# Kernel optimization log

Hardware: AMD Instinct MI355X
Metric: run time of the kernel (lower is better)

The kernel has to match this reference:

```python
import jax, jax.numpy as jnp
import numpy as np

N = 50000      # nodes
E = 800000     # edges (before self-loops)
IN = 128       # in_channels
HID = 32       # hidden_channels
H = 4          # heads (hidden layers)
H_LAST = 6     # heads of final conv (concat=False -> mean)
OUT = 2        # out_channels
NEG = 0.2      # LeakyReLU slope in GATConv


def setup_inputs() -> dict:
    key = jax.random.key(0)
    ks = jax.random.split(key, 24)
    r = lambda k, s, sc=0.1: (jax.random.normal(k, s, jnp.float32) * sc)
    inp = {
        "x": jax.random.normal(ks[0], (N, IN), jnp.float32),
        "edge_index": jax.random.randint(ks[1], (2, E), 0, N, dtype=jnp.int32),
        "edge_attr": jax.random.normal(ks[2], (E, 1), jnp.float32),  # ignored by GATConv (edge_dim=None)
        # layer 0: GATConv(IN -> HID, heads=H, concat) + Linear(IN -> HID*H)
        "c0_W": r(ks[3], (IN, H * HID)), "c0_as": r(ks[4], (H, HID)), "c0_ad": r(ks[5], (H, HID)), "c0_b": jnp.zeros((H * HID,), jnp.float32),
        "l0_W": r(ks[6], (IN, H * HID)), "l0_b": jnp.zeros((H * HID,), jnp.float32),
        # layer 1 (middle): GATConv(HID*H -> HID, heads=H) + Linear(HID*H -> HID*H)
        "c1_W": r(ks[7], (H * HID, H * HID)), "c1_as": r(ks[8], (H, HID)), "c1_ad": r(ks[9], (H, HID)), "c1_b": jnp.zeros((H * HID,), jnp.float32),
        "l1_W": r(ks[10], (H * HID, H * HID)), "l1_b": jnp.zeros((H * HID,), jnp.float32),
        # layer 2 (last): GATConv(HID*H -> OUT, heads=H_LAST, concat=False) + Linear(HID*H -> OUT)
        "c2_W": r(ks[11], (H * HID, H_LAST * OUT)), "c2_as": r(ks[12], (H_LAST, OUT)), "c2_ad": r(ks[13], (H_LAST, OUT)), "c2_b": jnp.zeros((OUT,), jnp.float32),
        "l2_W": r(ks[14], (H * HID, OUT)), "l2_b": jnp.zeros((OUT,), jnp.float32),
    }
    return inp


def gat_conv(x, src, dst, W, a_src, a_dst, b, heads, ch, concat):
    n = x.shape[0]
    xw = (x @ W).reshape(n, heads, ch)                      # [N,H,C]
    al_s = jnp.einsum('nhc,hc->nh', xw, a_src)              # [N,H]
    al_d = jnp.einsum('nhc,hc->nh', xw, a_dst)
    alpha = jax.nn.leaky_relu(al_s[src] + al_d[dst], NEG)   # [E,H]
    # segment softmax over edges sharing the same destination node
    m = jax.ops.segment_max(alpha, dst, num_segments=n)
    e = jnp.exp(alpha - m[dst])
    s = jax.ops.segment_sum(e, dst, num_segments=n)
    coef = e / s[dst]                                       # [E,H]
    out = jax.ops.segment_sum(xw[src] * coef[:, :, None], dst, num_segments=n)  # [N,H,C]
    out = out.reshape(n, heads * ch) if concat else out.mean(axis=1)
    return out + b


def reference(x, edge_index, edge_attr,
              c0_W, c0_as, c0_ad, c0_b, l0_W, l0_b,
              c1_W, c1_as, c1_ad, c1_b, l1_W, l1_b,
              c2_W, c2_as, c2_ad, c2_b, l2_W, l2_b):
    n = x.shape[0]
    loops = jnp.arange(n, dtype=edge_index.dtype)  # GATConv add_self_loops=True
    src = jnp.concatenate([edge_index[0], loops])
    dst = jnp.concatenate([edge_index[1], loops])
    # edge_attr is ignored: GATConv built without edge_dim has lin_edge=None
    h = jax.nn.relu(gat_conv(x, src, dst, c0_W, c0_as, c0_ad, c0_b, H, HID, True) + x @ l0_W + l0_b)
    h = jax.nn.relu(gat_conv(h, src, dst, c1_W, c1_as, c1_ad, c1_b, H, HID, True) + h @ l1_W + l1_b)
    out = gat_conv(h, src, dst, c2_W, c2_as, c2_ad, c2_b, H_LAST, OUT, False) + h @ l2_W + l2_b
    return out
```

## Files before the change

kernel.cpp:

```cpp
#include <hip/hip_runtime.h>
#include <hip/hip_bf16.h>


#define NEG_SLOPE 0.2f
#define SC_CHUNK 4096
#define CAP 64

typedef __attribute__((ext_vector_type(8))) short short8;
typedef __attribute__((ext_vector_type(4))) float floatx4;

static __device__ __forceinline__ float leaky(float x) {
    return x > 0.f ? x : NEG_SLOPE * x;
}

static __device__ __forceinline__ unsigned short f2bf(float f) {
    unsigned int u = __float_as_uint(f);
    u = (u + 0x7fffu + ((u >> 16) & 1u)) >> 16;
    return (unsigned short)u;
}

static __device__ __forceinline__ unsigned int pack_bf2(float lo, float hi) {
    return (unsigned int)f2bf(lo) | ((unsigned int)f2bf(hi) << 16);
}

static __device__ __forceinline__ float bflo(unsigned int u) {
    return __uint_as_float(u << 16);
}
static __device__ __forceinline__ float bfhi(unsigned int u) {
    return __uint_as_float(u & 0xffff0000u);
}

__global__ __launch_bounds__(256) void k_bucket(
    const int* __restrict__ ei, int E, int N, int rs,
    int* __restrict__ cnt, int* __restrict__ col) {
    int lo = blockIdx.x * rs, hi = lo + rs;
    int base = blockIdx.y * SC_CHUNK;
    int ET = E + N;
#pragma unroll 4
    for (int o = threadIdx.x; o < SC_CHUNK; o += 256) {
        int e = base + o;
        if (e >= ET) break;
        int d = (e < E) ? ei[E + e] : (e - E);
        if (d < lo || d >= hi) continue;
        int s = (e < E) ? ei[e] : d;
        int pos = atomicAdd(&cnt[d], 1);
        if (pos < CAP) col[(d << 6) + pos] = s;
    }
}


__global__ void k_conv_x(const float* __restrict__ x, unsigned short* __restrict__ Ab,
                         int N, int Mpad) {
    int t = blockIdx.x * 256 + threadIdx.x;
    if (t >= Mpad * 32) return;
    int r = t >> 5;
    float4 v = make_float4(0.f, 0.f, 0.f, 0.f);
    if (r < N) v = ((const float4*)x)[t];
    ushort4 o;
    o.x = f2bf(v.x); o.y = f2bf(v.y); o.z = f2bf(v.z); o.w = f2bf(v.w);
    ((ushort4*)Ab)[t] = o;
}

__global__ void k_conv_w(const float* W0, unsigned short* T0,
                         const float* W1, unsigned short* T1,
                         const float* W2, unsigned short* T2,
                         const float* W3, unsigned short* T3,
                         const float* c2W, const float* l2W, unsigned short* WT5) {
    int t = blockIdx.x * 256 + threadIdx.x;
    if (blockIdx.y == 4) {
        if (t >= 2048) return;
        int n = t >> 7, k = t & 127;
        float v = 0.f;
        if (n < 12) v = c2W[k * 12 + n];
        else if (n < 14) v = l2W[k * 2 + (n - 12)];
        WT5[n * 128 + k] = f2bf(v);
        return;
    }
    const float* W; unsigned short* T;
    switch (blockIdx.y) {
        case 0: W = W0; T = T0; break;
        case 1: W = W1; T = T1; break;
        case 2: W = W2; T = T2; break;
        default: W = W3; T = T3; break;
    }
    int n = t >> 7, k = t & 127;
    T[n * 128 + k] = f2bf(W[k * 128 + n]);
}

__global__ __launch_bounds__(256) void k_gemm_mfma(
    const unsigned short* __restrict__ Ab,
    const unsigned short* __restrict__ W1T,
    unsigned int* __restrict__ XWb,
    const float* __restrict__ a_s, const float* __restrict__ a_d,
    float4* __restrict__ ALS4, float4* __restrict__ ALD4,
    const unsigned short* __restrict__ W2T,
    const float* __restrict__ b2,
    unsigned short* __restrict__ Hsb,
    int M) {
    int which = blockIdx.y;
    const unsigned short* WT = which ? W2T : W1T;
    int row0 = blockIdx.x * 64;
    int w = threadIdx.x >> 6, lane = threadIdx.x & 63;
    int m = lane & 15, q = lane >> 4;

    const short8* A8 = (const short8*)Ab;
    const short8* W8 = (const short8*)WT;

    floatx4 acc[8];
#pragma unroll
    for (int ct = 0; ct < 8; ct++) acc[ct] = (floatx4){0.f, 0.f, 0.f, 0.f};

    int arow = row0 + w * 16 + m;
#pragma unroll
    for (int ks = 0; ks < 4; ks++) {
        short8 afrag = A8[arow * 16 + ks * 4 + q];
#pragma unroll
        for (int ct = 0; ct < 8; ct++) {
            short8 bfrag = W8[(ct * 16 + m) * 16 + ks * 4 + q];
            acc[ct] = __builtin_amdgcn_mfma_f32_16x16x32_bf16(afrag, bfrag, acc[ct], 0, 0, 0);
        }
    }

    int crow0 = row0 + w * 16 + q * 4;
    if (which) {
#pragma unroll
        for (int ct = 0; ct < 8; ct++) {
            int gc = ct * 16 + m;
            float bias = b2[gc];
#pragma unroll
            for (int r = 0; r < 4; r++) {
                int gr = crow0 + r;
                if (gr < M) Hsb[gr * 128 + gc] = f2bf(acc[ct][r] + bias);
            }
        }
    } else {
#pragma unroll
        for (int ct = 0; ct < 4; ct++) {
#pragma unroll
            for (int r = 0; r < 4; r++) {
                int gr = crow0 + r;
                if (gr < M)
                    XWb[gr * 64 + ct * 16 + m] = pack_bf2(acc[ct][r], acc[ct + 4][r]);
            }
        }
        float sv[4][4], dv[4][4];
#pragma unroll
        for (int h = 0; h < 4; h++) {
            float as0 = a_s[h * 32 + m], as1 = a_s[h * 32 + 16 + m];
            float ad0 = a_d[h * 32 + m], ad1 = a_d[h * 32 + 16 + m];
#pragma unroll
            for (int r = 0; r < 4; r++) {
                sv[h][r] = acc[2 * h][r] * as0 + acc[2 * h + 1][r] * as1;
                dv[h][r] = acc[2 * h][r] * ad0 + acc[2 * h + 1][r] * ad1;
            }
        }
#pragma unroll
        for (int off = 8; off >= 1; off >>= 1) {
#pragma unroll
            for (int h = 0; h < 4; h++)
#pragma unroll
                for (int r = 0; r < 4; r++) {
                    sv[h][r] += __shfl_xor(sv[h][r], off);
                    dv[h][r] += __shfl_xor(dv[h][r], off);
                }
        }
        if (m == 0) {
#pragma unroll
            for (int r = 0; r < 4; r++) {
                int gr = crow0 + r;
                if (gr < M) {
                    ALS4[gr] = make_float4(sv[0][r], sv[1][r], sv[2][r], sv[3][r]);
                    ALD4[gr] = make_float4(dv[0][r], dv[1][r], dv[2][r], dv[3][r]);
                }
            }
        }
    }
}

__global__ __launch_bounds__(256) void k_gemm_small(
    const unsigned short* __restrict__ Ab,
    const unsigned short* __restrict__ WT5,
    const float* __restrict__ c2as, const float* __restrict__ c2ad,
    const float* __restrict__ l2b,
    float* __restrict__ L2D, float* __restrict__ ALD2,
    float* __restrict__ out, int M) {
    int w = threadIdx.x >> 6, lane = threadIdx.x & 63;
    int m = lane & 15, q = lane >> 4;
    const short8* A8 = (const short8*)Ab;
    const short8* W8 = (const short8*)WT5;
    floatx4 acc = (floatx4){0.f, 0.f, 0.f, 0.f};
    int arow = blockIdx.x * 64 + w * 16 + m;
#pragma unroll
    for (int ks = 0; ks < 4; ks++) {
        short8 afrag = A8[arow * 16 + ks * 4 + q];
        short8 bfrag = W8[m * 16 + ks * 4 + q];
        acc = __builtin_amdgcn_mfma_f32_16x16x32_bf16(afrag, bfrag, acc, 0, 0, 0);
    }
    float asm_ = (m < 12) ? c2as[m] : 0.f;
    float adm  = (m < 12) ? c2ad[m] : 0.f;
    int crow0 = blockIdx.x * 64 + w * 16 + q * 4;
    float sc[4], dc[4];
#pragma unroll
    for (int r = 0; r < 4; r++) {
        sc[r] = acc[r] * asm_;
        dc[r] = acc[r] * adm;
    }
#pragma unroll
    for (int r = 0; r < 4; r++) {
        sc[r] += __shfl_xor(sc[r], 1);
        dc[r] += __shfl_xor(dc[r], 1);
    }
#pragma unroll
    for (int r = 0; r < 4; r++) {
        int gr = crow0 + r;
        if (gr >= M) continue;
        if (m < 12) {
            L2D[gr * 20 + m] = acc[r];
            if ((m & 1) == 0) {
                int h = m >> 1;
                L2D[gr * 20 + 12 + h] = sc[r];
                ALD2[gr * 8 + h] = dc[r];
            }
        } else if (m == 12) {
            out[gr * 2 + 0] = acc[r] + l2b[0];
        } else if (m == 13) {
            out[gr * 2 + 1] = acc[r] + l2b[1];
        }
    }
}

__global__ __launch_bounds__(256) void k_agg4(
    const int* __restrict__ cntv, const int* __restrict__ col,
    const uint4* __restrict__ XWb4,
    const float4* __restrict__ ALS4, const float4* __restrict__ ALD4,
    const float* __restrict__ cb,
    const unsigned short* __restrict__ Hsb, unsigned short* __restrict__ Hb, int N) {
    int wid = threadIdx.x >> 6, lane = threadIdx.x & 63;
    int node = blockIdx.x * 4 + wid;
    if (node >= N) return;
    int deg = cntv[node];
    if (deg > CAP) deg = CAP;
    int start = node << 6;
    int gq = lane >> 4, g = lane & 15;
    int hA = g >> 3;
    int cval = col[start + lane];
    float4 ad = ALD4[node];
    float adA = hA ? ad.y : ad.x;
    float adB = hA ? ad.w : ad.z;

    float a0 = 0.f, a1 = 0.f, a2 = 0.f, a3 = 0.f;
    float b0 = 0.f, b1 = 0.f, b2 = 0.f, b3 = 0.f;
    float sA = 0.f, sB = 0.f;

#define EDGE(sv)                                                       \
    {                                                                  \
        float4 as = ALS4[sv];                                          \
        uint4 u = XWb4[(size_t)(sv) * 16 + g];                         \
        float eA = __expf(leaky((hA ? as.y : as.x) + adA));            \
        float eB = __expf(leaky((hA ? as.w : as.z) + adB));            \
        sA += eA; sB += eB;                                            \
        a0 += eA * bflo(u.x); b0 += eB * bfhi(u.x);                    \
        a1 += eA * bflo(u.y); b1 += eB * bfhi(u.y);                    \
        a2 += eA * bflo(u.z); b2 += eB * bfhi(u.z);                    \
        a3 += eA * bflo(u.w); b3 += eB * bfhi(u.w);                    \
    }

    int i = 0;
    for (; i + 16 <= deg; i += 16) {
        int s0 = __shfl(cval, i + gq);
        int s1 = __shfl(cval, i + 4 + gq);
        int s2 = __shfl(cval, i + 8 + gq);
        int s3 = __shfl(cval, i + 12 + gq);
        EDGE(s0) EDGE(s1) EDGE(s2) EDGE(s3)
    }
    for (; i + 4 <= deg; i += 4) {
        int s0 = __shfl(cval, i + gq);
        EDGE(s0)
    }
    int rem = deg - i;
    if (rem > 0) {
        int s0 = __shfl(cval, i + (gq < rem ? gq : 0));
        if (gq < rem) EDGE(s0)
    }
#undef EDGE

#define RED2(v) { v += __shfl_xor(v, 16); v += __shfl_xor(v, 32); }
    RED2(sA) RED2(sB)
    RED2(a0) RED2(a1) RED2(a2) RED2(a3)
    RED2(b0) RED2(b1) RED2(b2) RED2(b3)
#undef RED2

    if (gq == 0) {
        float invA = 1.f / sA, invB = 1.f / sB;
        float4 cl = ((const float4*)cb)[g];
        float4 ch = ((const float4*)cb)[g + 16];
        uint2 skl = ((const uint2*)(Hsb + node * 128))[g];
        uint2 skh = ((const uint2*)(Hsb + node * 128 + 64))[g];
        float v0 = a0 * invA + cl.x + bflo(skl.x);
        float v1 = a1 * invA + cl.y + bfhi(skl.x);
        float v2 = a2 * invA + cl.z + bflo(skl.y);
        float v3 = a3 * invA + cl.w + bfhi(skl.y);
        float w0 = b0 * invB + ch.x + bflo(skh.x);
        float w1 = b1 * invB + ch.y + bfhi(skh.x);
        float w2 = b2 * invB + ch.z + bflo(skh.y);
        float w3 = b3 * invB + ch.w + bfhi(skh.y);
        v0 = v0 > 0.f ? v0 : 0.f;  v1 = v1 > 0.f ? v1 : 0.f;
        v2 = v2 > 0.f ? v2 : 0.f;  v3 = v3 > 0.f ? v3 : 0.f;
        w0 = w0 > 0.f ? w0 : 0.f;  w1 = w1 > 0.f ? w1 : 0.f;
        w2 = w2 > 0.f ? w2 : 0.f;  w3 = w3 > 0.f ? w3 : 0.f;
        uint2 ol, oh;
        ol.x = pack_bf2(v0, v1); ol.y = pack_bf2(v2, v3);
        oh.x = pack_bf2(w0, w1); oh.y = pack_bf2(w2, w3);
        ((uint2*)(Hb + node * 128))[g] = ol;
        ((uint2*)(Hb + node * 128 + 64))[g] = oh;
    }
}

__global__ __launch_bounds__(256) void k_agg2(
    const int* __restrict__ cntv, const int* __restrict__ col,
    const float4* __restrict__ L2D4,
    const float* __restrict__ ALD2,
    const float* __restrict__ c2b,
    float* __restrict__ out, int N) {
    int g = threadIdx.x >> 4, l = threadIdx.x & 15;
    int node = blockIdx.x * 16 + g;
    if (node >= N) return;
    int deg = cntv[node];
    if (deg > CAP) deg = CAP;
    int start = node << 6;

    int c0 = (l      < deg) ? col[start + l]      : -1;
    int c1 = (l + 16 < deg) ? col[start + l + 16] : -1;
    int c2 = (l + 32 < deg) ? col[start + l + 32] : -1;
    int c3 = (l + 48 < deg) ? col[start + l + 48] : -1;

    float ald[6];
    {
        float4 d03 = *(const float4*)(ALD2 + node * 8);
        float2 d45 = *(const float2*)(ALD2 + node * 8 + 4);
        ald[0] = d03.x; ald[1] = d03.y; ald[2] = d03.z; ald[3] = d03.w;
        ald[4] = d45.x; ald[5] = d45.y;
    }

    float se[6], a0[6], a1[6];
#pragma unroll
    for (int h = 0; h < 6; h++) { se[h] = 0.f; a0[h] = 0.f; a1[h] = 0.f; }

#define EDGE2(sv)                                                          \
    if ((sv) >= 0) {                                                       \
        float4 x03 = L2D4[(sv) * 5 + 0];                                   \
        float4 x47 = L2D4[(sv) * 5 + 1];                                   \
        float4 x8b = L2D4[(sv) * 5 + 2];                                   \
        float4 as03 = L2D4[(sv) * 5 + 3];                                  \
        float4 as45 = L2D4[(sv) * 5 + 4];                                  \
        float als[6] = {as03.x, as03.y, as03.z, as03.w, as45.x, as45.y};   \
        float xw[12] = {x03.x, x03.y, x03.z, x03.w, x47.x, x47.y, x47.z,   \
                        x47.w, x8b.x, x8b.y, x8b.z, x8b.w};                \
        _Pragma("unroll")                                                  \
        for (int h = 0; h < 6; h++) {                                      \
            float e = __expf(leaky(als[h] + ald[h]));                      \
            se[h] += e;                                                    \
            a0[h] += e * xw[2 * h];                                        \
            a1[h] += e * xw[2 * h + 1];                                    \
        }                                                                  \
    }

    EDGE2(c0) EDGE2(c1) EDGE2(c2) EDGE2(c3)
#undef EDGE2

#pragma unroll
    for (int m = 8; m >= 1; m >>= 1) {
#pragma unroll
        for (int h = 0; h < 6; h++) {
            se[h] += __shfl_xor(se[h], m);
            a0[h] += __shfl_xor(a0[h], m);
            a1[h] += __shfl_xor(a1[h], m);
        }
    }
    if (l == 0) {
        float o0 = 0.f, o1 = 0.f;
#pragma unroll
        for (int h = 0; h < 6; h++) {
            float inv = 1.f / se[h];
            o0 += a0[h] * inv;
            o1 += a1[h] * inv;
        }
        out[node * 2 + 0] += o0 * (1.f / 6.f) + c2b[0];
        out[node * 2 + 1] += o1 * (1.f / 6.f) + c2b[1];
    }
}


extern "C" void kernel_launch(void* const* d_in, const int* in_sizes, int n_in,
                              void* d_out, int out_size, void* d_ws, size_t ws_size,
                              hipStream_t stream) {
    const float* x   = (const float*)d_in[0];
    const int* ei    = (const int*)d_in[1];
    const float* c0W = (const float*)d_in[3];
    const float* c0as = (const float*)d_in[4];
    const float* c0ad = (const float*)d_in[5];
    const float* c0b = (const float*)d_in[6];
    const float* l0W = (const float*)d_in[7];
    const float* l0b = (const float*)d_in[8];
    const float* c1W = (const float*)d_in[9];
    const float* c1as = (const float*)d_in[10];
    const float* c1ad = (const float*)d_in[11];
    const float* c1b = (const float*)d_in[12];
    const float* l1W = (const float*)d_in[13];
    const float* l1b = (const float*)d_in[14];
    const float* c2W = (const float*)d_in[15];
    const float* c2as = (const float*)d_in[16];
    const float* c2ad = (const float*)d_in[17];
    const float* c2b = (const float*)d_in[18];
    const float* l2W = (const float*)d_in[19];
    const float* l2b = (const float*)d_in[20];
    float* out = (float*)d_out;

    const int N = in_sizes[0] / 128;
    const int E = in_sizes[1] / 2;
    const int ET = E + N;
    const int Mpad = (N + 63) & ~63;

    char* p = (char*)d_ws;
    auto alloc = [&](size_t bytes) -> void* {
        void* r = (void*)p;
        p += (bytes + 255) & ~(size_t)255;
        return r;
    };
    unsigned short* Hsb = (unsigned short*)alloc((size_t)N * 128 * 2);
    unsigned int* XWb = (unsigned int*)alloc((size_t)N * 64 * 4);
    unsigned short* Ab = (unsigned short*)alloc((size_t)Mpad * 128 * 2);
    unsigned short* W1T = (unsigned short*)alloc(128 * 128 * 2);
    unsigned short* W2T = (unsigned short*)alloc(128 * 128 * 2);
    unsigned short* W3T = (unsigned short*)alloc(128 * 128 * 2);
    unsigned short* W4T = (unsigned short*)alloc(128 * 128 * 2);
    unsigned short* WT5 = (unsigned short*)alloc(16 * 128 * 2);
    float* ALS = (float*)alloc((size_t)N * 4 * 4);
    float* ALD = (float*)alloc((size_t)N * 8 * 4);
    float* L2D = (float*)alloc((size_t)N * 20 * 4);
    int* cnt    = (int*)alloc((size_t)N * 4);
    int* col    = (int*)alloc((size_t)N * CAP * 4);

    hipMemsetAsync(cnt, 0, (size_t)N * 4, stream);
    int rs = (N + 7) / 8;
    dim3 bgrid(8, (ET + SC_CHUNK - 1) / SC_CHUNK);
    k_bucket<<<bgrid, 256, 0, stream>>>(ei, E, N, rs, cnt, col);

    k_conv_x<<<(Mpad * 32 + 255) / 256, 256, 0, stream>>>(x, Ab, N, Mpad);
    dim3 wgrid(64, 5);
    k_conv_w<<<wgrid, 256, 0, stream>>>(c0W, W1T, l0W, W2T, c1W, W3T, l1W, W4T,
                                        c2W, l2W, WT5);

    dim3 ggrid(Mpad / 64, 2);
    int nwb = (N + 3) / 4;

    k_gemm_mfma<<<ggrid, 256, 0, stream>>>(Ab, W1T, XWb, c0as, c0ad,
                                           (float4*)ALS, (float4*)ALD,
                                           W2T, l0b, Hsb, N);
    k_agg4<<<nwb, 256, 0, stream>>>(cnt, col, (const uint4*)XWb,
                                    (const float4*)ALS, (const float4*)ALD,
                                    c0b, Hsb, Ab, N);

    k_gemm_mfma<<<ggrid, 256, 0, stream>>>(Ab, W3T, XWb, c1as, c1ad,
                                           (float4*)ALS, (float4*)ALD,
                                           W4T, l1b, Hsb, N);
    k_agg4<<<nwb, 256, 0, stream>>>(cnt, col, (const uint4*)XWb,
                                    (const float4*)ALS, (const float4*)ALD,
                                    c1b, Hsb, Ab, N);

    k_gemm_small<<<Mpad / 64, 256, 0, stream>>>(Ab, WT5, c2as, c2ad, l2b,
                                                L2D, ALD, out, N);
    k_agg2<<<(N + 15) / 16, 256, 0, stream>>>(cnt, col, (const float4*)L2D,
                                              ALD, c2b, out, N);
}
```

Measured before the change: 332.1 us.

## Fuse weight conversion into bucketing and x conversion into first GEMM

Weight transposition and bf16 conversion now run in an extra row of blocks of the edge-bucketing kernel, and the standalone x-to-bf16 kernel is removed. The first GEMM instead reads fp32 x directly and converts the A fragments in registers. This drops two kernel launches and one full write and read of the converted x. The aggregation kernel also issues its bias and skip-connection loads before the edge loop so their latency overlaps the gather. The cost is that the first GEMM reads twice as many input bytes, and x is read once per column block.

```diff
diff --git a/kernel.cpp b/kernel.cpp
--- a/kernel.cpp
+++ b/kernel.cpp
@@ -30,9 +30,44 @@
     return __uint_as_float(u & 0xffff0000u);
 }
 
+static __device__ __forceinline__ short8 frag_from_f32(const float* p) {
+    float4 f0 = ((const float4*)p)[0];
+    float4 f1 = ((const float4*)p)[1];
+    short8 r;
+    r[0] = (short)f2bf(f0.x); r[1] = (short)f2bf(f0.y);
+    r[2] = (short)f2bf(f0.z); r[3] = (short)f2bf(f0.w);
+    r[4] = (short)f2bf(f1.x); r[5] = (short)f2bf(f1.y);
+    r[6] = (short)f2bf(f1.z); r[7] = (short)f2bf(f1.w);
+    return r;
+}
+
 __global__ __launch_bounds__(256) void k_bucket(
     const int* __restrict__ ei, int E, int N, int rs,
-    int* __restrict__ cnt, int* __restrict__ col) {
+    int* __restrict__ cnt, int* __restrict__ col,
+    const float* __restrict__ W0, unsigned short* __restrict__ T0,
+    const float* __restrict__ W1, unsigned short* __restrict__ T1,
+    const float* __restrict__ W2, unsigned short* __restrict__ T2,
+    const float* __restrict__ W3, unsigned short* __restrict__ T3,
+    const float* __restrict__ c2W, const float* __restrict__ l2W,
+    unsigned short* __restrict__ WT5) {
+    if (blockIdx.y == gridDim.y - 1) {
+        int tid = blockIdx.x * 256 + threadIdx.x;
+        for (int j = tid; j < 65536; j += 2048) {
+            int wsel = j >> 14, t = j & 16383;
+            int n = t >> 7, k = t & 127;
+            const float* W = (wsel == 0) ? W0 : (wsel == 1) ? W1 : (wsel == 2) ? W2 : W3;
+            unsigned short* T = (wsel == 0) ? T0 : (wsel == 1) ? T1 : (wsel == 2) ? T2 : T3;
+            T[n * 128 + k] = f2bf(W[k * 128 + n]);
+        }
+        {
+            int n = tid >> 7, k = tid & 127;
+            float v = 0.f;
+            if (n < 12) v = c2W[k * 12 + n];
+            else if (n < 14) v = l2W[k * 2 + (n - 12)];
+            WT5[n * 128 + k] = f2bf(v);
+        }
+        return;
+    }
     int lo = blockIdx.x * rs, hi = lo + rs;
     int base = blockIdx.y * SC_CHUNK;
     int ET = E + N;
@@ -48,46 +83,8 @@
     }
 }
 
-
-__global__ void k_conv_x(const float* __restrict__ x, unsigned short* __restrict__ Ab,
-                         int N, int Mpad) {
-    int t = blockIdx.x * 256 + threadIdx.x;
-    if (t >= Mpad * 32) return;
-    int r = t >> 5;
-    float4 v = make_float4(0.f, 0.f, 0.f, 0.f);
-    if (r < N) v = ((const float4*)x)[t];
-    ushort4 o;
-    o.x = f2bf(v.x); o.y = f2bf(v.y); o.z = f2bf(v.z); o.w = f2bf(v.w);
-    ((ushort4*)Ab)[t] = o;
-}
-
-__global__ void k_conv_w(const float* W0, unsigned short* T0,
-                         const float* W1, unsigned short* T1,
-                         const float* W2, unsigned short* T2,
-                         const float* W3, unsigned short* T3,
-                         const float* c2W, const float* l2W, unsigned short* WT5) {
-    int t = blockIdx.x * 256 + threadIdx.x;
-    if (blockIdx.y == 4) {
-        if (t >= 2048) return;
-        int n = t >> 7, k = t & 127;
-        float v = 0.f;
-        if (n < 12) v = c2W[k * 12 + n];
-        else if (n < 14) v = l2W[k * 2 + (n - 12)];
-        WT5[n * 128 + k] = f2bf(v);
-        return;
-    }
-    const float* W; unsigned short* T;
-    switch (blockIdx.y) {
-        case 0: W = W0; T = T0; break;
-        case 1: W = W1; T = T1; break;
-        case 2: W = W2; T = T2; break;
-        default: W = W3; T = T3; break;
-    }
-    int n = t >> 7, k = t & 127;
-    T[n * 128 + k] = f2bf(W[k * 128 + n]);
-}
-
 __global__ __launch_bounds__(256) void k_gemm_mfma(
+    const float* __restrict__ x0,
     const unsigned short* __restrict__ Ab,
     const unsigned short* __restrict__ W1T,
     unsigned int* __restrict__ XWb,
@@ -111,9 +108,11 @@
     for (int ct = 0; ct < 8; ct++) acc[ct] = (floatx4){0.f, 0.f, 0.f, 0.f};
 
     int arow = row0 + w * 16 + m;
+    int lrow = (arow < M) ? arow : (M - 1);
 #pragma unroll
     for (int ks = 0; ks < 4; ks++) {
-        short8 afrag = A8[arow * 16 + ks * 4 + q];
+        short8 afrag = x0 ? frag_from_f32(x0 + (size_t)lrow * 128 + (ks * 4 + q) * 8)
+                          : A8[arow * 16 + ks * 4 + q];
 #pragma unroll
         for (int ct = 0; ct < 8; ct++) {
             short8 bfrag = W8[(ct * 16 + m) * 16 + ks * 4 + q];
@@ -244,6 +243,10 @@
     int gq = lane >> 4, g = lane & 15;
     int hA = g >> 3;
     int cval = col[start + lane];
+    float4 cl = ((const float4*)cb)[g];
+    float4 ch = ((const float4*)cb)[g + 16];
+    uint2 skl = ((const uint2*)(Hsb + node * 128))[g];
+    uint2 skh = ((const uint2*)(Hsb + node * 128 + 64))[g];
     float4 ad = ALD4[node];
     float adA = hA ? ad.y : ad.x;
     float adB = hA ? ad.w : ad.z;
@@ -292,10 +295,6 @@
 
     if (gq == 0) {
         float invA = 1.f / sA, invB = 1.f / sB;
-        float4 cl = ((const float4*)cb)[g];
-        float4 ch = ((const float4*)cb)[g + 16];
-        uint2 skl = ((const uint2*)(Hsb + node * 128))[g];
-        uint2 skh = ((const uint2*)(Hsb + node * 128 + 64))[g];
         float v0 = a0 * invA + cl.x + bflo(skl.x);
         float v1 = a1 * invA + cl.y + bfhi(skl.x);
         float v2 = a2 * invA + cl.z + bflo(skl.y);
@@ -443,25 +442,23 @@
 
     hipMemsetAsync(cnt, 0, (size_t)N * 4, stream);
     int rs = (N + 7) / 8;
-    dim3 bgrid(8, (ET + SC_CHUNK - 1) / SC_CHUNK);
-    k_bucket<<<bgrid, 256, 0, stream>>>(ei, E, N, rs, cnt, col);
-
-    k_conv_x<<<(Mpad * 32 + 255) / 256, 256, 0, stream>>>(x, Ab, N, Mpad);
-    dim3 wgrid(64, 5);
-    k_conv_w<<<wgrid, 256, 0, stream>>>(c0W, W1T, l0W, W2T, c1W, W3T, l1W, W4T,
+    int chunks = (ET + SC_CHUNK - 1) / SC_CHUNK;
+    dim3 bgrid(8, chunks + 1);
+    k_bucket<<<bgrid, 256, 0, stream>>>(ei, E, N, rs, cnt, col,
+                                        c0W, W1T, l0W, W2T, c1W, W3T, l1W, W4T,
                                         c2W, l2W, WT5);
 
     dim3 ggrid(Mpad / 64, 2);
     int nwb = (N + 3) / 4;
 
-    k_gemm_mfma<<<ggrid, 256, 0, stream>>>(Ab, W1T, XWb, c0as, c0ad,
+    k_gemm_mfma<<<ggrid, 256, 0, stream>>>(x, Ab, W1T, XWb, c0as, c0ad,
                                            (float4*)ALS, (float4*)ALD,
                                            W2T, l0b, Hsb, N);
     k_agg4<<<nwb, 256, 0, stream>>>(cnt, col, (const uint4*)XWb,
                                     (const float4*)ALS, (const float4*)ALD,
                                     c0b, Hsb, Ab, N);
 
-    k_gemm_mfma<<<ggrid, 256, 0, stream>>>(Ab, W3T, XWb, c1as, c1ad,
+    k_gemm_mfma<<<ggrid, 256, 0, stream>>>(nullptr, Ab, W3T, XWb, c1as, c1ad,
                                            (float4*)ALS, (float4*)ALD,
                                            W4T, l1b, Hsb, N);
     k_agg4<<<nwb, 256, 0, stream>>>(cnt, col, (const uint4*)XWb,
```

Result: faster. 325.2 us (-2.1%).
